# Performance work log

Measured on AMD Instinct MI355X. Metric: run time of the kernel, lower is better.

## Reference

```python
import jax, jax.numpy as jnp
import numpy as np

N_NODES = 20000
N_FEAT = 10
EDGE_DIM = 6
D = 256
H = 8
C = D // H  # 32 per-head channels for gat1/gat2
B = 2048
E = 320000
NEG = 0.2        # LeakyReLU slope in GATConv attention
BN_EPS = 1e-5


def _bn_eval(x, g, b):
    # BatchNorm1d in eval mode with fresh buffers: running_mean=0, running_var=1
    return g * x * (1.0 / np.sqrt(1.0 + BN_EPS)) + b


def _gat(x, src, dst, edge_attr, W, a_src, a_dst, We, a_e, bias, heads, out_ch, n):
    # PyG GATConv with edge_dim: shared src/dst linear, per-head additive attention
    xp = (x @ W).reshape(n, heads, out_ch)                       # [N,H,C]
    al_s = jnp.einsum('nhc,hc->nh', xp, a_src)                   # [N,H]
    al_d = jnp.einsum('nhc,hc->nh', xp, a_dst)                   # [N,H]
    ep = (edge_attr @ We).reshape(-1, heads, out_ch)             # [E,H,C]
    al_e = jnp.einsum('ehc,hc->eh', ep, a_e)                     # [E,H]
    alpha = jax.nn.leaky_relu(al_s[src] + al_d[dst] + al_e, NEG)  # [E,H]
    # segment softmax over incoming edges of each dst node
    amax = jax.ops.segment_max(alpha, dst, num_segments=n)
    amax = jnp.where(jnp.isfinite(amax), amax, 0.0)
    ex = jnp.exp(alpha - amax[dst])
    den = jax.ops.segment_sum(ex, dst, num_segments=n)
    w = ex / (den[dst] + 1e-16)
    out = jax.ops.segment_sum(xp[src] * w[..., None], dst, num_segments=n)
    return out.reshape(n, heads * out_ch) + bias


def setup_inputs():
    key = jax.random.key(0)
    ks = iter(jax.random.split(key, 40))
    def rn(shape, scale=0.05):
        return jax.random.normal(next(ks), shape, dtype=jnp.float32) * scale
    inp = {}
    inp['current_node_ids'] = jax.random.randint(next(ks), (B,), 0, N_NODES)
    inp['network_features'] = jax.random.normal(next(ks), (B, N_FEAT), dtype=jnp.float32)
    inp['edge_index'] = jax.random.randint(next(ks), (2, E), 0, N_NODES)
    inp['edge_attr'] = jax.random.normal(next(ks), (E, EDGE_DIM), dtype=jnp.float32)
    inp['emb'] = rn((N_NODES, D), 1.0)
    inp['net_w1'] = rn((N_FEAT, D)); inp['net_b1'] = jnp.zeros((D,), jnp.float32)
    inp['net_g1'] = jnp.ones((D,), jnp.float32); inp['net_be1'] = jnp.zeros((D,), jnp.float32)
    inp['net_w2'] = rn((D, D)); inp['net_b2'] = jnp.zeros((D,), jnp.float32)
    inp['net_g2'] = jnp.ones((D,), jnp.float32); inp['net_be2'] = jnp.zeros((D,), jnp.float32)
    for i, (h, c) in enumerate([(H, C), (H, C), (1, D)], start=1):
        inp[f'gat{i}_W'] = rn((D, h * c))
        inp[f'gat{i}_as'] = rn((h, c)); inp[f'gat{i}_ad'] = rn((h, c))
        inp[f'gat{i}_We'] = rn((EDGE_DIM, h * c)); inp[f'gat{i}_ae'] = rn((h, c))
        inp[f'gat{i}_b'] = jnp.zeros((h * c,), jnp.float32)
    inp['fus_w'] = rn((2 * D, D)); inp['fus_b'] = jnp.zeros((D,), jnp.float32)
    inp['fus_g'] = jnp.ones((D,), jnp.float32); inp['fus_be'] = jnp.zeros((D,), jnp.float32)
    inp['cls_w'] = rn((D, N_NODES)); inp['cls_b'] = jnp.zeros((N_NODES,), jnp.float32)
    return inp


def reference(current_node_ids, network_features, edge_index, edge_attr, emb,
              net_w1, net_b1, net_g1, net_be1, net_w2, net_b2, net_g2, net_be2,
              gat1_W, gat1_as, gat1_ad, gat1_We, gat1_ae, gat1_b,
              gat2_W, gat2_as, gat2_ad, gat2_We, gat2_ae, gat2_b,
              gat3_W, gat3_as, gat3_ad, gat3_We, gat3_ae, gat3_b,
              fus_w, fus_b, fus_g, fus_be, cls_w, cls_b):
    src, dst = edge_index[0], edge_index[1]
    n = emb.shape[0]
    x = jax.nn.relu(_gat(emb, src, dst, edge_attr, gat1_W, gat1_as, gat1_ad, gat1_We, gat1_ae, gat1_b, H, C, n))
    x = jax.nn.relu(_gat(x, src, dst, edge_attr, gat2_W, gat2_as, gat2_ad, gat2_We, gat2_ae, gat2_b, H, C, n))
    x = _gat(x, src, dst, edge_attr, gat3_W, gat3_as, gat3_ad, gat3_We, gat3_ae, gat3_b, 1, D, n)
    node_emb = x[current_node_ids]                               # [B,D]
    h1 = jax.nn.relu(_bn_eval(network_features @ net_w1 + net_b1, net_g1, net_be1))
    net_emb = jax.nn.relu(_bn_eval(h1 @ net_w2 + net_b2, net_g2, net_be2))
    combined = jnp.concatenate([node_emb, net_emb], axis=1)      # [B,2D]
    fused = jax.nn.relu(_bn_eval(combined @ fus_w + fus_b, fus_g, fus_be))
    return fused @ cls_w + cls_b                                 # [B, N_NODES]
```

## Files before the change

### kernel.cpp

```cpp
#include <hip/hip_runtime.h>

#define NEG_SLOPE 0.2f
static constexpr float BN_INV = 0.9999950000374997f;

typedef __bf16 bf16x8 __attribute__((ext_vector_type(8)));
typedef float  f32x4  __attribute__((ext_vector_type(4)));

__device__ inline float4 bf4f(ushort4 u){
  float4 r;
  r.x = __uint_as_float((unsigned)u.x << 16);
  r.y = __uint_as_float((unsigned)u.y << 16);
  r.z = __uint_as_float((unsigned)u.z << 16);
  r.w = __uint_as_float((unsigned)u.w << 16);
  return r;
}
__device__ inline ushort4 f4bf(float4 v){
  ushort4 u;
  u.x = __builtin_bit_cast(unsigned short, (__bf16)v.x);
  u.y = __builtin_bit_cast(unsigned short, (__bf16)v.y);
  u.z = __builtin_bit_cast(unsigned short, (__bf16)v.z);
  u.w = __builtin_bit_cast(unsigned short, (__bf16)v.w);
  return u;
}

__global__ void hist_kernel(const int* __restrict__ dst, int* __restrict__ cnt, int E){
  int e = blockIdx.x*256 + threadIdx.x;
  if (e < E) atomicAdd(&cnt[dst[e]], 1);
}

__global__ __launch_bounds__(1024) void scan1_kernel(int* __restrict__ cnt_cursor,
                                                     int* __restrict__ offs,
                                                     int* __restrict__ bsum, int n){
  __shared__ int wsum[16];
  int tid = threadIdx.x, lane = tid & 63, wv = tid >> 6;
  int i = blockIdx.x*1024 + tid;
  int v = (i < n) ? cnt_cursor[i] : 0;
  int x = v;
#pragma unroll
  for (int off = 1; off < 64; off <<= 1){
    int t = __shfl_up(x, off);
    if (lane >= off) x += t;
  }
  if (lane == 63) wsum[wv] = x;
  __syncthreads();
  int y = (lane < 16) ? wsum[lane] : 0;
#pragma unroll
  for (int off = 1; off < 16; off <<= 1){
    int t = __shfl_up(y, off);
    if (lane >= off) y += t;
  }
  int excl  = (wv == 0) ? 0 : __shfl(y, wv - 1);
  int total = __shfl(y, 15);
  int inc = excl + x;
  if (i < n){ offs[i+1] = inc; cnt_cursor[i] = inc - v; }
  if (tid == 0) bsum[blockIdx.x] = total;
}

__global__ void scan2_kernel(int* __restrict__ bsum, int nb){
  int lane = threadIdx.x;
  int v = (lane < nb) ? bsum[lane] : 0;
  int x = v;
#pragma unroll
  for (int off = 1; off < 64; off <<= 1){
    int t = __shfl_up(x, off);
    if (lane >= off) x += t;
  }
  if (lane < nb) bsum[lane] = x - v;
}

__global__ __launch_bounds__(1024) void scan3_kernel(int* __restrict__ offs, int* __restrict__ cursor,
                                                     const int* __restrict__ bsum, int n){
  int i = blockIdx.x*1024 + threadIdx.x;
  int base = bsum[blockIdx.x];
  if (i < n){ offs[i+1] += base; cursor[i] += base; }
  if (i == 0) offs[0] = 0;
}

__global__ void scatter_kernel(const int* __restrict__ src, const int* __restrict__ dst,
                               const float* __restrict__ ea, int* __restrict__ cursor,
                               int* __restrict__ perm_src, float* __restrict__ ea_perm, int E){
  int e = blockIdx.x*256 + threadIdx.x;
  if (e >= E) return;
  int d = dst[e];
  int pos = atomicAdd(&cursor[d], 1);
  perm_src[pos] = src[e];
#pragma unroll
  for (int k = 0; k < 6; ++k) ea_perm[(size_t)pos*6 + k] = ea[(size_t)e*6 + k];
}

__global__ void foldm_all_kernel(const float* __restrict__ We1, const float* __restrict__ ae1,
                                 const float* __restrict__ We2, const float* __restrict__ ae2,
                                 const float* __restrict__ We3, const float* __restrict__ ae3,
                                 float* __restrict__ M){
  int t = threadIdx.x;
  if (t < 96){
    const float* We = (t < 48) ? We1 : We2;
    const float* ae = (t < 48) ? ae1 : ae2;
    int u = t % 48, k = u / 8, h = u % 8;
    float s = 0.f;
    for (int c = 0; c < 32; ++c) s += We[k*256 + h*32 + c] * ae[h*32 + c];
    M[t] = s;
  } else if (t < 102){
    int k = t - 96;
    float s = 0.f;
    for (int c = 0; c < 256; ++c) s += We3[k*256 + c] * ae3[c];
    M[t] = s;
  }
}

template<bool USE_BIAS, bool USE_BN, bool USE_RELU, typename OutT>
__global__ __launch_bounds__(256) void gemm_kernel(
    const float* __restrict__ A, const float* __restrict__ W,
    const float* __restrict__ bias, const float* __restrict__ gam, const float* __restrict__ bet,
    OutT* __restrict__ C, int M, int N, int K)
{
  __shared__ float As[32][68];
  __shared__ float Bs[32][64];
  int tid = threadIdx.x;
  int tx = tid & 15, ty = tid >> 4;
  int bn0 = blockIdx.x * 64, bm0 = blockIdx.y * 64;
  float acc[4][4] = {};
  for (int k0 = 0; k0 < K; k0 += 32){
    int kk = tid & 31, mm0 = tid >> 5;
#pragma unroll
    for (int r = 0; r < 8; ++r){
      int ml = mm0 + r*8;
      int m = bm0 + ml;
      As[kk][ml] = (m < M) ? A[(size_t)m*K + k0 + kk] : 0.f;
    }
    int nn = tid & 63, kb = tid >> 6;
#pragma unroll
    for (int r = 0; r < 8; ++r){
      int kl = kb + r*4;
      int n = bn0 + nn;
      Bs[kl][nn] = (n < N) ? W[(size_t)(k0 + kl)*N + n] : 0.f;
    }
    __syncthreads();
#pragma unroll
    for (int k = 0; k < 32; ++k){
      float4 a4 = *reinterpret_cast<const float4*>(&As[k][ty*4]);
      float4 b4 = *reinterpret_cast<const float4*>(&Bs[k][tx*4]);
      acc[0][0] += a4.x*b4.x; acc[0][1] += a4.x*b4.y; acc[0][2] += a4.x*b4.z; acc[0][3] += a4.x*b4.w;
      acc[1][0] += a4.y*b4.x; acc[1][1] += a4.y*b4.y; acc[1][2] += a4.y*b4.z; acc[1][3] += a4.y*b4.w;
      acc[2][0] += a4.z*b4.x; acc[2][1] += a4.z*b4.y; acc[2][2] += a4.z*b4.z; acc[2][3] += a4.z*b4.w;
      acc[3][0] += a4.w*b4.x; acc[3][1] += a4.w*b4.y; acc[3][2] += a4.w*b4.z; acc[3][3] += a4.w*b4.w;
    }
    __syncthreads();
  }
#pragma unroll
  for (int i = 0; i < 4; ++i){
    int m = bm0 + ty*4 + i;
    if (m < M){
#pragma unroll
      for (int j = 0; j < 4; ++j){
        int n = bn0 + tx*4 + j;
        if (n < N){
          float c = acc[i][j];
          if (USE_BIAS) c += bias[n];
          if (USE_BN)   c = gam[n]*c*BN_INV + bet[n];
          if (USE_RELU) c = fmaxf(c, 0.f);
          C[(size_t)m*N + n] = (OutT)c;
        }
      }
    }
  }
}

__global__ void wtrans_kernel(const float* __restrict__ W, __bf16* __restrict__ Wt, int K, int N){
  __shared__ float tile[32][33];
  int n0 = blockIdx.x*32, k0 = blockIdx.y*32;
  int t = threadIdx.x;
  int nl = t & 31, kl = t >> 5;
#pragma unroll
  for (int r = 0; r < 4; ++r)
    tile[kl + r*8][nl] = W[(size_t)(k0 + kl + r*8)*N + n0 + nl];
  __syncthreads();
  int nl2 = t >> 3, kc = (t & 7)*4;
#pragma unroll
  for (int j = 0; j < 4; ++j)
    Wt[(size_t)(n0 + nl2)*K + k0 + kc + j] = (__bf16)tile[kc + j][nl2];
}

__global__ void wtrans3_kernel(const float* __restrict__ W0, const float* __restrict__ W1,
                               const float* __restrict__ W2, __bf16* __restrict__ Wt){
  __shared__ float tile[32][33];
  const float* W = (blockIdx.z == 0) ? W0 : (blockIdx.z == 1) ? W1 : W2;
  __bf16* D = Wt + (size_t)blockIdx.z * 65536;
  int n0 = blockIdx.x*32, k0 = blockIdx.y*32;
  int t = threadIdx.x;
  int nl = t & 31, kl = t >> 5;
#pragma unroll
  for (int r = 0; r < 4; ++r)
    tile[kl + r*8][nl] = W[(size_t)(k0 + kl + r*8)*256 + n0 + nl];
  __syncthreads();
  int nl2 = t >> 3, kc = (t & 7)*4;
#pragma unroll
  for (int j = 0; j < 4; ++j)
    D[(size_t)(n0 + nl2)*256 + k0 + kc + j] = (__bf16)tile[kc + j][nl2];
}

template<bool USE_BIAS, bool AF32, int ALSD, typename OutT>
__global__ __launch_bounds__(256) void mfma_gemm_kernel(
    const void* __restrict__ Aptr, const __bf16* __restrict__ Bt,
    const float* __restrict__ bias, OutT* __restrict__ C, int M, int N, int K,
    const float* __restrict__ a_s, const float* __restrict__ a_d,
    float* __restrict__ als, float* __restrict__ ald)
{
  const __bf16* Ab = (const __bf16*)Aptr;
  const float*  Af = (const float*) Aptr;
  __shared__ __bf16 As[128*72];
  __shared__ __bf16 Bs[128*72];
  int tid = threadIdx.x;
  int lane = tid & 63, w = tid >> 6;
  int quad = lane >> 4, l16 = lane & 15;
  int wm = (w & 1) * 64, wn = (w >> 1) * 64;
  int bn0 = blockIdx.x * 128, bm0 = blockIdx.y * 128;
  f32x4 acc[4][4] = {};
  for (int k0 = 0; k0 < K; k0 += 64){
#pragma unroll
    for (int p = 0; p < 4; ++p){
      int idx = p*256 + tid;
      int row = idx >> 3, ch = idx & 7;
      uint4 av;
      if constexpr (AF32){
        av = make_uint4(0,0,0,0);
        int m = bm0 + row;
        if (m < M){
          const float4* A4 = reinterpret_cast<const float4*>(&Af[(size_t)m*K + k0 + ch*8]);
          float4 x0 = A4[0], x1 = A4[1];
          ushort4 u0 = f4bf(x0), u1 = f4bf(x1);
          av = make_uint4((unsigned)u0.x | ((unsigned)u0.y << 16),
                          (unsigned)u0.z | ((unsigned)u0.w << 16),
                          (unsigned)u1.x | ((unsigned)u1.y << 16),
                          (unsigned)u1.z | ((unsigned)u1.w << 16));
        }
      } else {
        av = *reinterpret_cast<const uint4*>(&Ab[(size_t)(bm0 + row)*K + k0 + ch*8]);
      }
      *reinterpret_cast<uint4*>(&As[row*72 + ch*8]) = av;
      int n = bn0 + row;
      uint4 bv = make_uint4(0,0,0,0);
      if (n < N) bv = *reinterpret_cast<const uint4*>(&Bt[(size_t)n*K + k0 + ch*8]);
      *reinterpret_cast<uint4*>(&Bs[row*72 + ch*8]) = bv;
    }
    __syncthreads();
#pragma unroll
    for (int s = 0; s < 2; ++s){
      bf16x8 af[4], bfr[4];
#pragma unroll
      for (int t4 = 0; t4 < 4; ++t4){
        af[t4]  = *reinterpret_cast<const bf16x8*>(&As[(wm + t4*16 + l16)*72 + s*32 + quad*8]);
        bfr[t4] = *reinterpret_cast<const bf16x8*>(&Bs[(wn + t4*16 + l16)*72 + s*32 + quad*8]);
      }
#pragma unroll
      for (int mt = 0; mt < 4; ++mt)
#pragma unroll
        for (int nt = 0; nt < 4; ++nt)
          acc[mt][nt] = __builtin_amdgcn_mfma_f32_16x16x32_bf16(af[mt], bfr[nt], acc[mt][nt], 0, 0, 0);
    }
    __syncthreads();
  }
#pragma unroll
  for (int mt = 0; mt < 4; ++mt){
#pragma unroll
    for (int nt = 0; nt < 4; ++nt){
      int n = bn0 + wn + nt*16 + l16;
      if (n < N){
        float bv = USE_BIAS ? bias[n] : 0.f;
#pragma unroll
        for (int r = 0; r < 4; ++r){
          int m = bm0 + wm + mt*16 + quad*4 + r;
          if (m < M) C[(size_t)m*N + n] = (OutT)(acc[mt][nt][r] + bv);
        }
      }
    }
  }
  if constexpr (ALSD == 8){
    float av4[4], dv4[4];
#pragma unroll
    for (int nt = 0; nt < 4; ++nt){
      int n = bn0 + wn + nt*16 + l16;
      av4[nt] = a_s[n];
      dv4[nt] = a_d[n];
    }
    int hb = (bn0 + wn) >> 5;
#pragma unroll
    for (int mt = 0; mt < 4; ++mt){
#pragma unroll
      for (int r = 0; r < 4; ++r){
        float s0 = acc[mt][0][r]*av4[0] + acc[mt][1][r]*av4[1];
        float s1 = acc[mt][2][r]*av4[2] + acc[mt][3][r]*av4[3];
        float d0 = acc[mt][0][r]*dv4[0] + acc[mt][1][r]*dv4[1];
        float d1 = acc[mt][2][r]*dv4[2] + acc[mt][3][r]*dv4[3];
#pragma unroll
        for (int off = 1; off < 16; off <<= 1){
          s0 += __shfl_xor(s0, off); s1 += __shfl_xor(s1, off);
          d0 += __shfl_xor(d0, off); d1 += __shfl_xor(d1, off);
        }
        if (l16 == 0){
          int m = bm0 + wm + mt*16 + quad*4 + r;
          if (m < M){
            als[m*8 + hb]     = s0; als[m*8 + hb + 1] = s1;
            ald[m*8 + hb]     = d0; ald[m*8 + hb + 1] = d1;
          }
        }
      }
    }
  }
}

template<int HH>
__global__ void alsd_kernel(const __bf16* __restrict__ xp, const float* __restrict__ a_s,
                            const float* __restrict__ a_d, float* __restrict__ als,
                            float* __restrict__ ald, int Nn){
  int gid = blockIdx.x*blockDim.x + threadIdx.x;
  int wave = gid >> 6, lane = threadIdx.x & 63;
  if (wave >= Nn) return;
  float4 xv = bf4f(reinterpret_cast<const ushort4*>(xp)[(size_t)wave*64 + lane]);
  float4 av = reinterpret_cast<const float4*>(a_s)[lane];
  float4 dv = reinterpret_cast<const float4*>(a_d)[lane];
  float ps = xv.x*av.x + xv.y*av.y + xv.z*av.z + xv.w*av.w;
  float pd = xv.x*dv.x + xv.y*dv.y + xv.z*dv.z + xv.w*dv.w;
  if constexpr (HH == 8){
    ps += __shfl_xor(ps,1); pd += __shfl_xor(pd,1);
    ps += __shfl_xor(ps,2); pd += __shfl_xor(pd,2);
    ps += __shfl_xor(ps,4); pd += __shfl_xor(pd,4);
    if ((lane & 7) == 0){
      als[wave*8 + (lane>>3)] = ps;
      ald[wave*8 + (lane>>3)] = pd;
    }
  } else {
#pragma unroll
    for (int off = 1; off < 64; off <<= 1){ ps += __shfl_xor(ps,off); pd += __shfl_xor(pd,off); }
    if (lane == 0){ als[wave] = ps; ald[wave] = pd; }
  }
}

template<int HH>
__global__ void agg_kernel(const int* __restrict__ offs, const int* __restrict__ perm_src,
                           const float* __restrict__ ea_perm, const float* __restrict__ Mf,
                           const float* __restrict__ als, const float* __restrict__ ald,
                           const __bf16* __restrict__ xp, const float* __restrict__ bias,
                           __bf16* __restrict__ out, int Nn, int do_relu){
  int gid = blockIdx.x*blockDim.x + threadIdx.x;
  int wave = gid >> 6, lane = threadIdx.x & 63;
  if (wave >= Nn) return;
  int beg = offs[wave], end = offs[wave+1];
  int hsel = (HH == 8) ? (lane >> 3) : 0;

  float mk[6];
#pragma unroll
  for (int k = 0; k < 6; ++k) mk[k] = Mf[k*HH + hsel];
  float aldv = ald[(size_t)wave*HH + hsel];

  const ushort4* X4 = reinterpret_cast<const ushort4*>(xp);
  float4 acc = make_float4(0.f,0.f,0.f,0.f);
  float den = 0.f;

  int i = beg;
  for (; i + 3 < end; i += 4){
    int s0 = perm_src[i], s1 = perm_src[i+1], s2 = perm_src[i+2], s3 = perm_src[i+3];
    float a0 = als[(size_t)s0*HH + hsel] + aldv;
    float a1 = als[(size_t)s1*HH + hsel] + aldv;
    float a2 = als[(size_t)s2*HH + hsel] + aldv;
    float a3 = als[(size_t)s3*HH + hsel] + aldv;
#pragma unroll
    for (int k = 0; k < 6; ++k){
      a0 += ea_perm[(size_t)i*6 + k]     * mk[k];
      a1 += ea_perm[(size_t)(i+1)*6 + k] * mk[k];
      a2 += ea_perm[(size_t)(i+2)*6 + k] * mk[k];
      a3 += ea_perm[(size_t)(i+3)*6 + k] * mk[k];
    }
    a0 = (a0 > 0.f) ? a0 : NEG_SLOPE*a0;
    a1 = (a1 > 0.f) ? a1 : NEG_SLOPE*a1;
    a2 = (a2 > 0.f) ? a2 : NEG_SLOPE*a2;
    a3 = (a3 > 0.f) ? a3 : NEG_SLOPE*a3;
    float e0 = __expf(a0), e1 = __expf(a1), e2 = __expf(a2), e3 = __expf(a3);
    den += (e0 + e1) + (e2 + e3);
    float4 x0 = bf4f(X4[(size_t)s0*64 + lane]);
    float4 x1 = bf4f(X4[(size_t)s1*64 + lane]);
    float4 x2 = bf4f(X4[(size_t)s2*64 + lane]);
    float4 x3 = bf4f(X4[(size_t)s3*64 + lane]);
    acc.x += x0.x*e0 + x1.x*e1 + x2.x*e2 + x3.x*e3;
    acc.y += x0.y*e0 + x1.y*e1 + x2.y*e2 + x3.y*e3;
    acc.z += x0.z*e0 + x1.z*e1 + x2.z*e2 + x3.z*e3;
    acc.w += x0.w*e0 + x1.w*e1 + x2.w*e2 + x3.w*e3;
  }
  for (; i < end; ++i){
    int s = perm_src[i];
    float a = als[(size_t)s*HH + hsel] + aldv;
#pragma unroll
    for (int k = 0; k < 6; ++k) a += ea_perm[(size_t)i*6 + k] * mk[k];
    a = (a > 0.f) ? a : NEG_SLOPE*a;
    float e = __expf(a);
    den += e;
    float4 xv = bf4f(X4[(size_t)s*64 + lane]);
    acc.x += xv.x*e; acc.y += xv.y*e; acc.z += xv.z*e; acc.w += xv.w*e;
  }

  float r = 1.f / (den + 1e-16f);
  float4 bv = reinterpret_cast<const float4*>(bias)[lane];
  acc.x = acc.x*r + bv.x; acc.y = acc.y*r + bv.y;
  acc.z = acc.z*r + bv.z; acc.w = acc.w*r + bv.w;
  if (do_relu){
    acc.x = fmaxf(acc.x,0.f); acc.y = fmaxf(acc.y,0.f);
    acc.z = fmaxf(acc.z,0.f); acc.w = fmaxf(acc.w,0.f);
  }
  reinterpret_cast<ushort4*>(out)[(size_t)wave*64 + lane] = f4bf(acc);
}

__global__ void h1_kernel(const float* __restrict__ nf, const float* __restrict__ w1,
                          const float* __restrict__ b1, const float* __restrict__ g,
                          const float* __restrict__ be, float* __restrict__ out){
  int b = blockIdx.x, j = threadIdx.x;
  float s = b1[j];
#pragma unroll
  for (int k = 0; k < 10; ++k) s += nf[b*10 + k] * w1[k*256 + j];
  s = g[j]*s*BN_INV + be[j];
  out[b*256 + j] = fmaxf(s, 0.f);
}

__global__ void gather_kernel(const int* __restrict__ ids, const __bf16* __restrict__ gat3out,
                              const float* __restrict__ netemb, float* __restrict__ comb){
  int b = blockIdx.x, t = threadIdx.x;
  float4 v;
  if (t < 64) v = bf4f(reinterpret_cast<const ushort4*>(gat3out)[(size_t)ids[b]*64 + t]);
  else        v = reinterpret_cast<const float4*>(netemb)[(size_t)b*64 + (t-64)];
  reinterpret_cast<float4*>(comb)[(size_t)b*128 + t] = v;
}

extern "C" void kernel_launch(void* const* d_in, const int* in_sizes, int n_in,
                              void* d_out, int out_size, void* d_ws, size_t ws_size,
                              hipStream_t stream)
{
  const int*   ids   = (const int*)  d_in[0];
  const float* nf    = (const float*)d_in[1];
  const int*   eidx  = (const int*)  d_in[2];
  const float* eattr = (const float*)d_in[3];
  const float* emb   = (const float*)d_in[4];
  const float* w1    = (const float*)d_in[5];
  const float* b1    = (const float*)d_in[6];
  const float* g1    = (const float*)d_in[7];
  const float* be1   = (const float*)d_in[8];
  const float* w2    = (const float*)d_in[9];
  const float* b2    = (const float*)d_in[10];
  const float* g2    = (const float*)d_in[11];
  const float* be2   = (const float*)d_in[12];
  const float* gW[3]  = {(const float*)d_in[13], (const float*)d_in[19], (const float*)d_in[25]};
  const float* gas[3] = {(const float*)d_in[14], (const float*)d_in[20], (const float*)d_in[26]};
  const float* gad[3] = {(const float*)d_in[15], (const float*)d_in[21], (const float*)d_in[27]};
  const float* gWe[3] = {(const float*)d_in[16], (const float*)d_in[22], (const float*)d_in[28]};
  const float* gae[3] = {(const float*)d_in[17], (const float*)d_in[23], (const float*)d_in[29]};
  const float* gb[3]  = {(const float*)d_in[18], (const float*)d_in[24], (const float*)d_in[30]};
  const float* fus_w  = (const float*)d_in[31];
  const float* fus_b  = (const float*)d_in[32];
  const float* fus_g  = (const float*)d_in[33];
  const float* fus_be = (const float*)d_in[34];
  const float* cls_w  = (const float*)d_in[35];
  const float* cls_b  = (const float*)d_in[36];

  const int E  = in_sizes[3] / 6;
  const int Nn = in_sizes[4] / 256;
  const int B  = in_sizes[0];
  const int Ncls = in_sizes[36];
  const int Npad = (Nn + 127) & ~127;
  const int* src = eidx;
  const int* dst = eidx + E;

  char* wbase = (char*)d_ws;
  size_t woff = 0;
  auto carve = [&](size_t bytes)->void*{
    void* p = wbase + woff;
    woff = (woff + bytes + 255) & ~(size_t)255;
    return p;
  };
  int*    offs     = (int*)   carve((size_t)(Nn+1)*4);
  int*    cursor   = (int*)   carve((size_t)Nn*4);
  int*    bsum     = (int*)   carve(64*4);
  int*    perm_src = (int*)   carve((size_t)E*4);
  float*  ea_perm  = (float*) carve((size_t)E*6*4);
  __bf16* xb0      = (__bf16*)carve((size_t)Npad*256*2);
  __bf16* xb1      = (__bf16*)carve((size_t)Npad*256*2);
  __bf16* xpb      = (__bf16*)carve((size_t)Npad*256*2);
  __bf16* gWt      = (__bf16*)carve((size_t)3*256*256*2);
  float*  als      = (float*) carve((size_t)Nn*8*4);
  float*  ald      = (float*) carve((size_t)Nn*8*4);
  float*  Mfold    = (float*) carve(128*4);
  float*  h1b      = (float*) carve((size_t)B*256*4);
  float*  netemb   = (float*) carve((size_t)B*256*4);
  float*  comb     = (float*) carve((size_t)B*512*4);
  __bf16* fusedb   = (__bf16*)carve((size_t)B*256*2);
  __bf16* clsWt    = (__bf16*)carve((size_t)Ncls*256*2);
  (void)ws_size; (void)n_in; (void)out_size;

  const int nb1024 = (Nn + 1023) / 1024;

  hipMemsetAsync(cursor, 0, (size_t)Nn*4, stream);
  hist_kernel<<<(E+255)/256, 256, 0, stream>>>(dst, cursor, E);
  scan1_kernel<<<nb1024, 1024, 0, stream>>>(cursor, offs, bsum, Nn);
  scan2_kernel<<<1, 64, 0, stream>>>(bsum, nb1024);
  scan3_kernel<<<nb1024, 1024, 0, stream>>>(offs, cursor, bsum, Nn);
  scatter_kernel<<<(E+255)/256, 256, 0, stream>>>(src, dst, eattr, cursor,
                                                  perm_src, ea_perm, E);

  foldm_all_kernel<<<1, 128, 0, stream>>>(gWe[0], gae[0], gWe[1], gae[1], gWe[2], gae[2], Mfold);
  wtrans3_kernel<<<dim3(8, 8, 3), 256, 0, stream>>>(gW[0], gW[1], gW[2], gWt);
  wtrans_kernel<<<dim3(Ncls/32, 256/32), 256, 0, stream>>>(cls_w, clsWt, 256, Ncls);

  dim3 mfma_grid_xp(2, Npad/128);
  int node_blocks = (Nn*64 + 255)/256;

  mfma_gemm_kernel<false, true, 8, __bf16><<<mfma_grid_xp, 256, 0, stream>>>(
      emb, gWt, nullptr, xpb, Nn, 256, 256, gas[0], gad[0], als, ald);
  agg_kernel<8><<<node_blocks, 256, 0, stream>>>(offs, perm_src, ea_perm, Mfold,
                                                 als, ald, xpb, gb[0], xb1, Nn, 1);
  mfma_gemm_kernel<false, false, 8, __bf16><<<mfma_grid_xp, 256, 0, stream>>>(
      xb1, gWt + 65536, nullptr, xpb, Nn, 256, 256, gas[1], gad[1], als, ald);
  agg_kernel<8><<<node_blocks, 256, 0, stream>>>(offs, perm_src, ea_perm, Mfold + 48,
                                                 als, ald, xpb, gb[1], xb0, Nn, 1);
  mfma_gemm_kernel<false, false, 0, __bf16><<<mfma_grid_xp, 256, 0, stream>>>(
      xb0, gWt + 131072, nullptr, xpb, Nn, 256, 256, nullptr, nullptr, nullptr, nullptr);
  alsd_kernel<1><<<node_blocks, 256, 0, stream>>>(xpb, gas[2], gad[2], als, ald, Nn);
  agg_kernel<1><<<node_blocks, 256, 0, stream>>>(offs, perm_src, ea_perm, Mfold + 96,
                                                 als, ald, xpb, gb[2], xb1, Nn, 0);

  h1_kernel<<<B, 256, 0, stream>>>(nf, w1, b1, g1, be1, h1b);
  gemm_kernel<true,true,true,float><<<dim3(4, B/64), 256, 0, stream>>>(
      h1b, w2, b2, g2, be2, netemb, B, 256, 256);

  gather_kernel<<<B, 128, 0, stream>>>(ids, xb1, netemb, comb);
  gemm_kernel<true,true,true,__bf16><<<dim3(4, B/64), 256, 0, stream>>>(
      comb, fus_w, fus_b, fus_g, fus_be, fusedb, B, 256, 512);
  mfma_gemm_kernel<true, false, 0, float><<<dim3((Ncls+127)/128, B/128), 256, 0, stream>>>(
      fusedb, clsWt, cls_b, (float*)d_out, B, Ncls, 256, nullptr, nullptr, nullptr, nullptr);
}
```

Measured before the change: 736.7 us.

## Aggregate final GAT layer only for queried nodes and write into combined buffer

The third GAT aggregation now runs only for the B queried node ids instead of all N nodes, writing straight into the concatenated buffer. This removes the separate gather kernel and lets the net-embedding GEMM write into the second half of the combined buffer through a new leading-dimension argument. The attention-fold kernel is merged into the weight-transpose launch as an extra grid slice, saving one launch. The output is unchanged because only rows at current_node_ids are consumed.

After: 711.3 us. 1.04x faster.

```diff
diff --git a/kernel.cpp b/kernel.cpp
--- a/kernel.cpp
+++ b/kernel.cpp
@@ -88,31 +88,11 @@
   for (int k = 0; k < 6; ++k) ea_perm[(size_t)pos*6 + k] = ea[(size_t)e*6 + k];
 }
 
-__global__ void foldm_all_kernel(const float* __restrict__ We1, const float* __restrict__ ae1,
-                                 const float* __restrict__ We2, const float* __restrict__ ae2,
-                                 const float* __restrict__ We3, const float* __restrict__ ae3,
-                                 float* __restrict__ M){
-  int t = threadIdx.x;
-  if (t < 96){
-    const float* We = (t < 48) ? We1 : We2;
-    const float* ae = (t < 48) ? ae1 : ae2;
-    int u = t % 48, k = u / 8, h = u % 8;
-    float s = 0.f;
-    for (int c = 0; c < 32; ++c) s += We[k*256 + h*32 + c] * ae[h*32 + c];
-    M[t] = s;
-  } else if (t < 102){
-    int k = t - 96;
-    float s = 0.f;
-    for (int c = 0; c < 256; ++c) s += We3[k*256 + c] * ae3[c];
-    M[t] = s;
-  }
-}
-
 template<bool USE_BIAS, bool USE_BN, bool USE_RELU, typename OutT>
 __global__ __launch_bounds__(256) void gemm_kernel(
     const float* __restrict__ A, const float* __restrict__ W,
     const float* __restrict__ bias, const float* __restrict__ gam, const float* __restrict__ bet,
-    OutT* __restrict__ C, int M, int N, int K)
+    OutT* __restrict__ C, int M, int N, int K, int LDC)
 {
   __shared__ float As[32][68];
   __shared__ float Bs[32][64];
@@ -159,7 +139,7 @@
           if (USE_BIAS) c += bias[n];
           if (USE_BN)   c = gam[n]*c*BN_INV + bet[n];
           if (USE_RELU) c = fmaxf(c, 0.f);
-          C[(size_t)m*N + n] = (OutT)c;
+          C[(size_t)m*LDC + n] = (OutT)c;
         }
       }
     }
@@ -182,7 +162,29 @@
 }
 
 __global__ void wtrans3_kernel(const float* __restrict__ W0, const float* __restrict__ W1,
-                               const float* __restrict__ W2, __bf16* __restrict__ Wt){
+                               const float* __restrict__ W2, __bf16* __restrict__ Wt,
+                               const float* __restrict__ We1, const float* __restrict__ ae1,
+                               const float* __restrict__ We2, const float* __restrict__ ae2,
+                               const float* __restrict__ We3, const float* __restrict__ ae3,
+                               float* __restrict__ M){
+  if (blockIdx.z == 3){
+    if (blockIdx.x != 0 || blockIdx.y != 0) return;
+    int t = threadIdx.x;
+    if (t < 96){
+      const float* We = (t < 48) ? We1 : We2;
+      const float* ae = (t < 48) ? ae1 : ae2;
+      int u = t % 48, k = u / 8, h = u % 8;
+      float s = 0.f;
+      for (int c = 0; c < 32; ++c) s += We[k*256 + h*32 + c] * ae[h*32 + c];
+      M[t] = s;
+    } else if (t < 102){
+      int k = t - 96;
+      float s = 0.f;
+      for (int c = 0; c < 256; ++c) s += We3[k*256 + c] * ae3[c];
+      M[t] = s;
+    }
+    return;
+  }
   __shared__ float tile[32][33];
   const float* W = (blockIdx.z == 0) ? W0 : (blockIdx.z == 1) ? W1 : W2;
   __bf16* D = Wt + (size_t)blockIdx.z * 65536;
@@ -309,10 +311,9 @@
   }
 }
 
-template<int HH>
-__global__ void alsd_kernel(const __bf16* __restrict__ xp, const float* __restrict__ a_s,
-                            const float* __restrict__ a_d, float* __restrict__ als,
-                            float* __restrict__ ald, int Nn){
+__global__ void alsd1_kernel(const __bf16* __restrict__ xp, const float* __restrict__ a_s,
+                             const float* __restrict__ a_d, float* __restrict__ als,
+                             float* __restrict__ ald, int Nn){
   int gid = blockIdx.x*blockDim.x + threadIdx.x;
   int wave = gid >> 6, lane = threadIdx.x & 63;
   if (wave >= Nn) return;
@@ -321,37 +322,26 @@
   float4 dv = reinterpret_cast<const float4*>(a_d)[lane];
   float ps = xv.x*av.x + xv.y*av.y + xv.z*av.z + xv.w*av.w;
   float pd = xv.x*dv.x + xv.y*dv.y + xv.z*dv.z + xv.w*dv.w;
-  if constexpr (HH == 8){
-    ps += __shfl_xor(ps,1); pd += __shfl_xor(pd,1);
-    ps += __shfl_xor(ps,2); pd += __shfl_xor(pd,2);
-    ps += __shfl_xor(ps,4); pd += __shfl_xor(pd,4);
-    if ((lane & 7) == 0){
-      als[wave*8 + (lane>>3)] = ps;
-      ald[wave*8 + (lane>>3)] = pd;
-    }
-  } else {
-#pragma unroll
-    for (int off = 1; off < 64; off <<= 1){ ps += __shfl_xor(ps,off); pd += __shfl_xor(pd,off); }
-    if (lane == 0){ als[wave] = ps; ald[wave] = pd; }
-  }
-}
-
-template<int HH>
-__global__ void agg_kernel(const int* __restrict__ offs, const int* __restrict__ perm_src,
-                           const float* __restrict__ ea_perm, const float* __restrict__ Mf,
-                           const float* __restrict__ als, const float* __restrict__ ald,
-                           const __bf16* __restrict__ xp, const float* __restrict__ bias,
-                           __bf16* __restrict__ out, int Nn, int do_relu){
+#pragma unroll
+  for (int off = 1; off < 64; off <<= 1){ ps += __shfl_xor(ps,off); pd += __shfl_xor(pd,off); }
+  if (lane == 0){ als[wave] = ps; ald[wave] = pd; }
+}
+
+__global__ void agg8_kernel(const int* __restrict__ offs, const int* __restrict__ perm_src,
+                            const float* __restrict__ ea_perm, const float* __restrict__ Mf,
+                            const float* __restrict__ als, const float* __restrict__ ald,
+                            const __bf16* __restrict__ xp, const float* __restrict__ bias,
+                            __bf16* __restrict__ out, int Nn){
   int gid = blockIdx.x*blockDim.x + threadIdx.x;
   int wave = gid >> 6, lane = threadIdx.x & 63;
   if (wave >= Nn) return;
   int beg = offs[wave], end = offs[wave+1];
-  int hsel = (HH == 8) ? (lane >> 3) : 0;
+  int hsel = lane >> 3;
 
   float mk[6];
 #pragma unroll
-  for (int k = 0; k < 6; ++k) mk[k] = Mf[k*HH + hsel];
-  float aldv = ald[(size_t)wave*HH + hsel];
+  for (int k = 0; k < 6; ++k) mk[k] = Mf[k*8 + hsel];
+  float aldv = ald[(size_t)wave*8 + hsel];
 
   const ushort4* X4 = reinterpret_cast<const ushort4*>(xp);
   float4 acc = make_float4(0.f,0.f,0.f,0.f);
@@ -360,10 +350,10 @@
   int i = beg;
   for (; i + 3 < end; i += 4){
     int s0 = perm_src[i], s1 = perm_src[i+1], s2 = perm_src[i+2], s3 = perm_src[i+3];
-    float a0 = als[(size_t)s0*HH + hsel] + aldv;
-    float a1 = als[(size_t)s1*HH + hsel] + aldv;
-    float a2 = als[(size_t)s2*HH + hsel] + aldv;
-    float a3 = als[(size_t)s3*HH + hsel] + aldv;
+    float a0 = als[(size_t)s0*8 + hsel] + aldv;
+    float a1 = als[(size_t)s1*8 + hsel] + aldv;
+    float a2 = als[(size_t)s2*8 + hsel] + aldv;
+    float a3 = als[(size_t)s3*8 + hsel] + aldv;
 #pragma unroll
     for (int k = 0; k < 6; ++k){
       a0 += ea_perm[(size_t)i*6 + k]     * mk[k];
@@ -388,7 +378,7 @@
   }
   for (; i < end; ++i){
     int s = perm_src[i];
-    float a = als[(size_t)s*HH + hsel] + aldv;
+    float a = als[(size_t)s*8 + hsel] + aldv;
 #pragma unroll
     for (int k = 0; k < 6; ++k) a += ea_perm[(size_t)i*6 + k] * mk[k];
     a = (a > 0.f) ? a : NEG_SLOPE*a;
@@ -400,13 +390,75 @@
 
   float r = 1.f / (den + 1e-16f);
   float4 bv = reinterpret_cast<const float4*>(bias)[lane];
+  acc.x = fmaxf(acc.x*r + bv.x, 0.f); acc.y = fmaxf(acc.y*r + bv.y, 0.f);
+  acc.z = fmaxf(acc.z*r + bv.z, 0.f); acc.w = fmaxf(acc.w*r + bv.w, 0.f);
+  reinterpret_cast<ushort4*>(out)[(size_t)wave*64 + lane] = f4bf(acc);
+}
+
+__global__ void agg1q_kernel(const int* __restrict__ ids, const int* __restrict__ offs,
+                             const int* __restrict__ perm_src, const float* __restrict__ ea_perm,
+                             const float* __restrict__ Mf, const float* __restrict__ als,
+                             const float* __restrict__ ald, const __bf16* __restrict__ xp,
+                             const float* __restrict__ bias, float* __restrict__ comb, int B){
+  int gid = blockIdx.x*blockDim.x + threadIdx.x;
+  int wave = gid >> 6, lane = threadIdx.x & 63;
+  if (wave >= B) return;
+  int node = ids[wave];
+  int beg = offs[node], end = offs[node+1];
+
+  float mk[6];
+#pragma unroll
+  for (int k = 0; k < 6; ++k) mk[k] = Mf[k];
+  float aldv = ald[node];
+
+  const ushort4* X4 = reinterpret_cast<const ushort4*>(xp);
+  float4 acc = make_float4(0.f,0.f,0.f,0.f);
+  float den = 0.f;
+
+  int i = beg;
+  for (; i + 3 < end; i += 4){
+    int s0 = perm_src[i], s1 = perm_src[i+1], s2 = perm_src[i+2], s3 = perm_src[i+3];
+    float a0 = als[s0] + aldv, a1 = als[s1] + aldv;
+    float a2 = als[s2] + aldv, a3 = als[s3] + aldv;
+#pragma unroll
+    for (int k = 0; k < 6; ++k){
+      a0 += ea_perm[(size_t)i*6 + k]     * mk[k];
+      a1 += ea_perm[(size_t)(i+1)*6 + k] * mk[k];
+      a2 += ea_perm[(size_t)(i+2)*6 + k] * mk[k];
+      a3 += ea_perm[(size_t)(i+3)*6 + k] * mk[k];
+    }
+    a0 = (a0 > 0.f) ? a0 : NEG_SLOPE*a0;
+    a1 = (a1 > 0.f) ? a1 : NEG_SLOPE*a1;
+    a2 = (a2 > 0.f) ? a2 : NEG_SLOPE*a2;
+    a3 = (a3 > 0.f) ? a3 : NEG_SLOPE*a3;
+    float e0 = __expf(a0), e1 = __expf(a1), e2 = __expf(a2), e3 = __expf(a3);
+    den += (e0 + e1) + (e2 + e3);
+    float4 x0 = bf4f(X4[(size_t)s0*64 + lane]);
+    float4 x1 = bf4f(X4[(size_t)s1*64 + lane]);
+    float4 x2 = bf4f(X4[(size_t)s2*64 + lane]);
+    float4 x3 = bf4f(X4[(size_t)s3*64 + lane]);
+    acc.x += x0.x*e0 + x1.x*e1 + x2.x*e2 + x3.x*e3;
+    acc.y += x0.y*e0 + x1.y*e1 + x2.y*e2 + x3.y*e3;
+    acc.z += x0.z*e0 + x1.z*e1 + x2.z*e2 + x3.z*e3;
+    acc.w += x0.w*e0 + x1.w*e1 + x2.w*e2 + x3.w*e3;
+  }
+  for (; i < end; ++i){
+    int s = perm_src[i];
+    float a = als[s] + aldv;
+#pragma unroll
+    for (int k = 0; k < 6; ++k) a += ea_perm[(size_t)i*6 + k] * mk[k];
+    a = (a > 0.f) ? a : NEG_SLOPE*a;
+    float e = __expf(a);
+    den += e;
+    float4 xv = bf4f(X4[(size_t)s*64 + lane]);
+    acc.x += xv.x*e; acc.y += xv.y*e; acc.z += xv.z*e; acc.w += xv.w*e;
+  }
+
+  float r = 1.f / (den + 1e-16f);
+  float4 bv = reinterpret_cast<const float4*>(bias)[lane];
   acc.x = acc.x*r + bv.x; acc.y = acc.y*r + bv.y;
   acc.z = acc.z*r + bv.z; acc.w = acc.w*r + bv.w;
-  if (do_relu){
-    acc.x = fmaxf(acc.x,0.f); acc.y = fmaxf(acc.y,0.f);
-    acc.z = fmaxf(acc.z,0.f); acc.w = fmaxf(acc.w,0.f);
-  }
-  reinterpret_cast<ushort4*>(out)[(size_t)wave*64 + lane] = f4bf(acc);
+  reinterpret_cast<float4*>(comb)[(size_t)wave*128 + lane] = acc;
 }
 
 __global__ void h1_kernel(const float* __restrict__ nf, const float* __restrict__ w1,
@@ -418,15 +470,6 @@
   for (int k = 0; k < 10; ++k) s += nf[b*10 + k] * w1[k*256 + j];
   s = g[j]*s*BN_INV + be[j];
   out[b*256 + j] = fmaxf(s, 0.f);
-}
-
-__global__ void gather_kernel(const int* __restrict__ ids, const __bf16* __restrict__ gat3out,
-                              const float* __restrict__ netemb, float* __restrict__ comb){
-  int b = blockIdx.x, t = threadIdx.x;
-  float4 v;
-  if (t < 64) v = bf4f(reinterpret_cast<const ushort4*>(gat3out)[(size_t)ids[b]*64 + t]);
-  else        v = reinterpret_cast<const float4*>(netemb)[(size_t)b*64 + (t-64)];
-  reinterpret_cast<float4*>(comb)[(size_t)b*128 + t] = v;
 }
 
 extern "C" void kernel_launch(void* const* d_in, const int* in_sizes, int n_in,
@@ -487,7 +530,6 @@
   float*  ald      = (float*) carve((size_t)Nn*8*4);
   float*  Mfold    = (float*) carve(128*4);
   float*  h1b      = (float*) carve((size_t)B*256*4);
-  float*  netemb   = (float*) carve((size_t)B*256*4);
   float*  comb     = (float*) carve((size_t)B*512*4);
   __bf16* fusedb   = (__bf16*)carve((size_t)B*256*2);
   __bf16* clsWt    = (__bf16*)carve((size_t)Ncls*256*2);
@@ -503,8 +545,9 @@
   scatter_kernel<<<(E+255)/256, 256, 0, stream>>>(src, dst, eattr, cursor,
                                                   perm_src, ea_perm, E);
 
-  foldm_all_kernel<<<1, 128, 0, stream>>>(gWe[0], gae[0], gWe[1], gae[1], gWe[2], gae[2], Mfold);
-  wtrans3_kernel<<<dim3(8, 8, 3), 256, 0, stream>>>(gW[0], gW[1], gW[2], gWt);
+  wtrans3_kernel<<<dim3(8, 8, 4), 256, 0, stream>>>(gW[0], gW[1], gW[2], gWt,
+                                                    gWe[0], gae[0], gWe[1], gae[1],
+                                                    gWe[2], gae[2], Mfold);
   wtrans_kernel<<<dim3(Ncls/32, 256/32), 256, 0, stream>>>(cls_w, clsWt, 256, Ncls);
 
   dim3 mfma_grid_xp(2, Npad/128);
@@ -512,25 +555,24 @@
 
   mfma_gemm_kernel<false, true, 8, __bf16><<<mfma_grid_xp, 256, 0, stream>>>(
       emb, gWt, nullptr, xpb, Nn, 256, 256, gas[0], gad[0], als, ald);
-  agg_kernel<8><<<node_blocks, 256, 0, stream>>>(offs, perm_src, ea_perm, Mfold,
-                                                 als, ald, xpb, gb[0], xb1, Nn, 1);
+  agg8_kernel<<<node_blocks, 256, 0, stream>>>(offs, perm_src, ea_perm, Mfold,
+                                               als, ald, xpb, gb[0], xb1, Nn);
   mfma_gemm_kernel<false, false, 8, __bf16><<<mfma_grid_xp, 256, 0, stream>>>(
       xb1, gWt + 65536, nullptr, xpb, Nn, 256, 256, gas[1], gad[1], als, ald);
-  agg_kernel<8><<<node_blocks, 256, 0, stream>>>(offs, perm_src, ea_perm, Mfold + 48,
-                                                 als, ald, xpb, gb[1], xb0, Nn, 1);
+  agg8_kernel<<<node_blocks, 256, 0, stream>>>(offs, perm_src, ea_perm, Mfold + 48,
+                                               als, ald, xpb, gb[1], xb0, Nn);
   mfma_gemm_kernel<false, false, 0, __bf16><<<mfma_grid_xp, 256, 0, stream>>>(
       xb0, gWt + 131072, nullptr, xpb, Nn, 256, 256, nullptr, nullptr, nullptr, nullptr);
-  alsd_kernel<1><<<node_blocks, 256, 0, stream>>>(xpb, gas[2], gad[2], als, ald, Nn);
-  agg_kernel<1><<<node_blocks, 256, 0, stream>>>(offs, perm_src, ea_perm, Mfold + 96,
-                                                 als, ald, xpb, gb[2], xb1, Nn, 0);
+  alsd1_kernel<<<node_blocks, 256, 0, stream>>>(xpb, gas[2], gad[2], als, ald, Nn);
+  agg1q_kernel<<<(B*64 + 255)/256, 256, 0, stream>>>(ids, offs, perm_src, ea_perm,
+                                                     Mfold + 96, als, ald, xpb, gb[2], comb, B);
 
   h1_kernel<<<B, 256, 0, stream>>>(nf, w1, b1, g1, be1, h1b);
   gemm_kernel<true,true,true,float><<<dim3(4, B/64), 256, 0, stream>>>(
-      h1b, w2, b2, g2, be2, netemb, B, 256, 256);
-
-  gather_kernel<<<B, 128, 0, stream>>>(ids, xb1, netemb, comb);
+      h1b, w2, b2, g2, be2, comb + 256, B, 256, 256, 512);
+
   gemm_kernel<true,true,true,__bf16><<<dim3(4, B/64), 256, 0, stream>>>(
-      comb, fus_w, fus_b, fus_g, fus_be, fusedb, B, 256, 512);
+      comb, fus_w, fus_b, fus_g, fus_be, fusedb, B, 256, 512, 256);
   mfma_gemm_kernel<true, false, 0, float><<<dim3((Ncls+127)/128, B/128), 256, 0, stream>>>(
       fusedb, clsWt, cls_b, (float*)d_out, B, Ncls, 256, nullptr, nullptr, nullptr, nullptr);
 }
```
